# Optimization experiments

Hardware: AMD Instinct MI355X
Metric: run time of the kernel (lower is better)

## Reference

```python
import jax, jax.numpy as jnp
import numpy as np

B, T, N, D = 4, 8, 128, 512
H = 8
DH = D // H            # 64
HALF = DH // 2         # 32
NUM_FEATS = 3
SH_HID = 16
NUM_COEFF = 4          # l=0 (1) + l=1 (3)
ROPE_BASE = 1000.0
EPS = 1e-6
Y0 = 0.28209479177387814   # 1/sqrt(4*pi)
Y1 = 0.4886025119029199    # sqrt(3/(4*pi))


def setup_inputs() -> dict:
    key = jax.random.key(0)
    ks = jax.random.split(key, 16)
    s = 0.02
    return {
        'x_0': jax.random.normal(ks[0], (B, T, N, D), jnp.float32),
        'v_0': jax.random.normal(ks[1], (B, T, N, D), jnp.float32),
        'concatenated_features': jax.random.normal(ks[2], (B, T, N, D), jnp.float32),
        'q_data': jax.random.normal(ks[3], (B, T, N, D), jnp.float32),
        'Wq': jax.random.normal(ks[4], (D, D), jnp.float32) * s,
        'bq': jnp.zeros((D,), jnp.float32),
        'Wkv': jax.random.normal(ks[5], (NUM_FEATS, D, 2 * D), jnp.float32) * s,
        'bkv': jnp.zeros((NUM_FEATS, 2 * D), jnp.float32),
        'Wo': jax.random.normal(ks[6], (D, D), jnp.float32) * s,
        'bo': jnp.zeros((D,), jnp.float32),
        'feature_weights': jax.random.normal(ks[7], (NUM_FEATS,), jnp.float32) * 0.1,
        'attention_denom': jnp.full((H,), float(DH), jnp.float32),
        'W1': jax.random.normal(ks[8], (NUM_COEFF, SH_HID), jnp.float32) * 0.3,
        'b1': jnp.zeros((SH_HID,), jnp.float32),
        'W2': jax.random.normal(ks[9], (SH_HID, SH_HID), jnp.float32) * 0.3,
        'b2': jnp.zeros((SH_HID,), jnp.float32),
        'W3': jax.random.normal(ks[10], (SH_HID, H), jnp.float32) * 0.3,
        'b3': jnp.zeros((H,), jnp.float32),
    }


def _rope(t):
    # t: [B, H, S, DH]; groups of N nodes share the same timestep, offsets = 0
    positions = jnp.repeat(jnp.arange(T, dtype=jnp.float32), N)  # [S]
    freqs = 1.0 / (ROPE_BASE ** (2.0 * jnp.arange(HALF, dtype=jnp.float32) / DH))
    angle = positions[:, None] * freqs[None, :]                  # [S, HALF]
    cos_t, sin_t = jnp.cos(angle), jnp.sin(angle)
    t1, t2 = t[..., 0::2], t[..., 1::2]
    r0 = t1 * cos_t - t2 * sin_t
    r1 = t1 * sin_t + t2 * cos_t
    return jnp.stack([r0, r1], axis=-1).reshape(t.shape)


def _sh_bias(coords3, W1, b1, W2, b2, W3, b3):
    # coords3: [B, S, 3] -> bias [B, H, S, S]
    rel = coords3[:, :, None, :] - coords3[:, None, :, :]        # [B,S,S,3]
    norm = jnp.linalg.norm(rel, axis=-1, keepdims=True)
    unit = rel / (norm + EPS)
    # e3nn l=1 component order is (y, z, x)
    sh = jnp.concatenate([
        jnp.full(unit.shape[:-1] + (1,), Y0, unit.dtype),
        Y1 * unit[..., jnp.array([1, 2, 0])],
    ], axis=-1)                                                  # [B,S,S,4]
    h = jax.nn.silu(sh @ W1 + b1)
    h = jax.nn.silu(h @ W2 + b2)
    bias = h @ W3 + b3                                           # [B,S,S,H]
    return jnp.transpose(bias, (0, 3, 1, 2))                     # [B,H,S,S]


def reference(x_0, v_0, concatenated_features, q_data, Wq, bq, Wkv, bkv, Wo, bo,
              feature_weights, attention_denom, W1, b1, W2, b2, W3, b3):
    S = T * N
    q = (q_data.reshape(B, S, D) @ Wq + bq).reshape(B, S, H, DH)
    q = _rope(jnp.transpose(q, (0, 2, 1, 3)))                    # [B,H,S,DH]

    bias = _sh_bias(x_0[..., :3].reshape(B, S, 3), W1, b1, W2, b2, W3, b3)
    gates = jax.nn.softmax(feature_weights)
    inv_denom = (1.0 / attention_denom)[None, :, None, None]

    out = jnp.zeros((B, H, S, DH), q.dtype)
    for i, feat in enumerate([x_0, v_0, concatenated_features]):
        kv = feat.reshape(B, S, D) @ Wkv[i] + bkv[i]             # [B,S,2D]
        k, v = kv[..., :D], kv[..., D:]
        k = _rope(jnp.transpose(k.reshape(B, S, H, DH), (0, 2, 1, 3)))
        v = jnp.transpose(v.reshape(B, S, H, DH), (0, 2, 1, 3))
        scores = jnp.einsum('bhqd,bhkd->bhqk', q, k) * inv_denom + bias
        attn = jax.nn.softmax(scores, axis=-1)                   # dropout=identity (eval)
        out = out + gates[i] * jnp.einsum('bhqk,bhkd->bhqd', attn, v)

    out = jnp.transpose(out, (0, 2, 1, 3)).reshape(B, S, D)
    return (out @ Wo + bo).reshape(B, T, N, D)
```

## Files before the change

### kernel.cpp

```cpp
#include <hip/hip_runtime.h>
#include <hip/hip_bf16.h>

typedef unsigned short u16;
typedef __attribute__((ext_vector_type(4))) float f32x4;
typedef __attribute__((ext_vector_type(8))) short v8s;
typedef __attribute__((ext_vector_type(4))) _Float16 h16x4;
typedef __attribute__((ext_vector_type(2))) unsigned int u32x2;

#define NB 4
#define NT 8
#define NN 128
#define ND 512
#define NH 8
#define NDH 64
#define NS 1024

static __device__ __forceinline__ u16 f2b(float f) {
  __hip_bfloat16 h = __float2bfloat16(f);
  return *reinterpret_cast<u16*>(&h);
}
static __device__ __forceinline__ float b2f(u16 u) {
  __hip_bfloat16 h;
  *reinterpret_cast<u16*>(&h) = u;
  return __bfloat162float(h);
}
static __device__ __forceinline__ unsigned int cvtpk(float lo, float hi) {
  unsigned int r;
  asm("v_cvt_pk_bf16_f32 %0, %1, %2" : "=v"(r) : "v"(lo), "v"(hi));
  return r;
}
static __device__ __forceinline__ void gl16(const u16* g, u16* l) {
  __builtin_amdgcn_global_load_lds(
      (const __attribute__((address_space(1))) unsigned int*)g,
      (__attribute__((address_space(3))) unsigned int*)l, 16, 0, 0);
}
static __device__ __forceinline__ f32x4 mfma16(h16x4 a, h16x4 b, f32x4 c) {
#if __has_builtin(__builtin_amdgcn_mfma_f32_16x16x16f16)
  return __builtin_amdgcn_mfma_f32_16x16x16f16(a, b, c, 0, 0, 0);
#else
  f32x4 d;
  asm volatile("v_mfma_f32_16x16x16_f16 %0, %1, %2, %3\n\ts_nop 7\n\ts_nop 7"
               : "=v"(d)
               : "v"(a), "v"(b), "v"(c));
  return d;
#endif
}
static __device__ __forceinline__ float frcp(float x) { return __builtin_amdgcn_rcpf(x); }
static __device__ __forceinline__ float fsqrt(float x) { return __builtin_amdgcn_sqrtf(x); }

__global__ void __launch_bounds__(256) cast4_kernel(const float* __restrict__ s0,
                                                    const float* __restrict__ s1,
                                                    const float* __restrict__ s2,
                                                    const float* __restrict__ s3,
                                                    u16* __restrict__ dst) {
  int blk = blockIdx.x;
  int seg = blk >> 10;
  const float* src = seg == 0 ? s0 : (seg == 1 ? s1 : (seg == 2 ? s2 : s3));
  int i = (blk & 1023) * 256 + threadIdx.x;
  const float4* s4 = reinterpret_cast<const float4*>(src) + (size_t)i * 2;
  float4 a = s4[0], b = s4[1];
  u16 r[8] = {f2b(a.x), f2b(a.y), f2b(a.z), f2b(a.w),
              f2b(b.x), f2b(b.y), f2b(b.z), f2b(b.w)};
  *reinterpret_cast<v8s*>(dst + (size_t)seg * 2097152 + (size_t)i * 8) =
      *reinterpret_cast<v8s*>(r);
}

__global__ void __launch_bounds__(256) transpose_cast_kernel(const float* __restrict__ W,
                                                             u16* __restrict__ Wt,
                                                             int K, int N) {
  __shared__ float t[32][33];
  int tx = threadIdx.x & 31, ty = threadIdx.x >> 5;
  int kb = blockIdx.y * 32, nb = blockIdx.x * 32;
#pragma unroll
  for (int i = 0; i < 4; i++) {
    int r = ty + i * 8;
    t[r][tx] = W[(size_t)(kb + r) * N + nb + tx];
  }
  __syncthreads();
#pragma unroll
  for (int i = 0; i < 4; i++) {
    int r = ty + i * 8;
    Wt[(size_t)(nb + r) * K + kb + tx] = f2b(t[tx][r]);
  }
}

__global__ void coords_kernel(const float* __restrict__ x0, float* __restrict__ c, int n) {
  int i = blockIdx.x * blockDim.x + threadIdx.x;
  if (i < n) {
    float4 v;
    v.x = x0[(size_t)i * ND + 0];
    v.y = x0[(size_t)i * ND + 1];
    v.z = x0[(size_t)i * ND + 2];
    v.w = 0.0f;
    reinterpret_cast<float4*>(c)[i] = v;
  }
}

__global__ void __launch_bounds__(256) gemm_kernel(const u16* __restrict__ A,
                                                   const u16* __restrict__ Wt,
                                                   const float* __restrict__ bias,
                                                   const float* __restrict__ dnm,
                                                   u16* __restrict__ outK,
                                                   u16* __restrict__ outV,
                                                   float* __restrict__ outF,
                                                   int M, int N, int K, int mode, int f) {
  __shared__ __align__(16) u16 sbuf[2 * 8192];
  int nt = N >> 7;
  int by = blockIdx.x / nt, bx = blockIdx.x % nt;
  int tid = threadIdx.x;
  int lane = tid & 63, wave = tid >> 6;
  int g = lane >> 4, li = lane & 15;
  int wr = (wave & 1) * 64, wc = (wave >> 1) * 64;
  f32x4 acc[4][4] = {};
  const u16* srcs[4];
  int dsts[4];
#pragma unroll
  for (int j = 0; j < 4; j++) {
    int c = wave * 4 + j;
    if (c < 8)
      srcs[j] = A + (size_t)(by * 128 + c * 16 + li) * K + g * 8;
    else
      srcs[j] = Wt + (size_t)(bx * 128 + (c - 8) * 16 + li) * K + g * 8;
    dsts[j] = c * 512 + lane * 8;
  }
  int nsteps = K >> 5;
#pragma unroll
  for (int j = 0; j < 4; j++) gl16(srcs[j], sbuf + dsts[j]);
  for (int t = 0; t < nsteps; t++) {
    int p = t & 1;
    if (t < nsteps - 1) {
#pragma unroll
      for (int j = 0; j < 4; j++)
        gl16(srcs[j] + (t + 1) * 32, sbuf + (p ^ 1) * 8192 + dsts[j]);
      asm volatile("s_waitcnt vmcnt(4)" ::: "memory");
    } else {
      asm volatile("s_waitcnt vmcnt(0)" ::: "memory");
    }
    __builtin_amdgcn_s_barrier();
    __builtin_amdgcn_sched_barrier(0);
    const u16* bufb = sbuf + p * 8192;
    v8s a[4], b[4];
#pragma unroll
    for (int mi = 0; mi < 4; mi++)
      a[mi] = *reinterpret_cast<const v8s*>(bufb + ((wr >> 4) + mi) * 512 + lane * 8);
#pragma unroll
    for (int ni = 0; ni < 4; ni++)
      b[ni] = *reinterpret_cast<const v8s*>(bufb + 4096 + ((wc >> 4) + ni) * 512 + lane * 8);
    __builtin_amdgcn_s_setprio(1);
#pragma unroll
    for (int mi = 0; mi < 4; mi++)
#pragma unroll
      for (int ni = 0; ni < 4; ni++)
        acc[mi][ni] = __builtin_amdgcn_mfma_f32_16x16x32_bf16(a[mi], b[ni], acc[mi][ni], 0, 0, 0);
    __builtin_amdgcn_s_setprio(0);
    __builtin_amdgcn_s_barrier();
  }
#pragma unroll
  for (int mi = 0; mi < 4; mi++)
#pragma unroll
    for (int ni = 0; ni < 4; ni++) {
      int n = bx * 128 + wc + ni * 16 + li;
      float bn = bias[n];
      int mbase = by * 128 + wr + mi * 16 + 4 * g;
      bool isv = (mode == 1) && (n >= 512);
      if (mode == 2) {
#pragma unroll
        for (int r = 0; r < 4; r++)
          outF[(size_t)(mbase + r) * N + n] = acc[mi][ni][r] + bn;
      } else if (!isv) {
        int d = n & 63, h = (n & 511) >> 6;
        int j = d >> 1;
        float freq = __expf(-(float)j * 0.21586735246819178f);
        float sca = (mode == 0) ? frcp(dnm[h]) : 1.0f;
#pragma unroll
        for (int r = 0; r < 4; r++) {
          int mrow = mbase + r;
          int b = mrow >> 10, s = mrow & 1023;
          float val = acc[mi][ni][r] + bn;
          float partner = __shfl_xor(val, 1);
          float ang = (float)(s >> 7) * freq;
          float sn = __sinf(ang), cs = __cosf(ang);
          float res = (n & 1) ? (partner * sn + val * cs) : (val * cs - partner * sn);
          res *= sca;
          size_t idx;
          if (mode == 0)
            idx = ((size_t)(b * NH + h) * NS + s) * NDH + d;
          else
            idx = ((size_t)((f * NB + b) * NH + h) * NS + s) * NDH + d;
          outK[idx] = f2b(res);
        }
      } else {
        int vd = n - 512;
        int h = vd >> 6, d = vd & 63;
        int b = mbase >> 10, s0 = mbase & 1023;
        u16 pk[4];
#pragma unroll
        for (int r = 0; r < 4; r++) pk[r] = f2b(acc[mi][ni][r] + bn);
        u16* dst = outV + ((size_t)((f * NB + b) * NH + h) * NDH + d) * NS + s0;
        *reinterpret_cast<ushort4*>(dst) = *reinterpret_cast<ushort4*>(pk);
      }
    }
}

__global__ void __launch_bounds__(256) bias_kernel(const float* __restrict__ coords,
                                                   const float* __restrict__ W1,
                                                   const float* __restrict__ b1,
                                                   const float* __restrict__ W2,
                                                   const float* __restrict__ b2,
                                                   const float* __restrict__ W3,
                                                   const float* __restrict__ b3,
                                                   u16* __restrict__ biasF) {
  int wave = threadIdx.x >> 6, lane = threadIdx.x & 63;
  int g = lane >> 4, li = lane & 15;
  int id = blockIdx.x * 4 + wave;
  int kt = id & 31, qt = (id >> 5) & 63, b = id >> 11;
  const float Y0 = 0.28209479177387814f;
  const float Y1 = 0.4886025119029199f;

  h16x4 A1 = {}, A2, A3;
#pragma unroll
  for (int r = 0; r < 4; r++) {
    A1[r] = (g == 0) ? (_Float16)W1[r * 16 + li] : (_Float16)0.0f;
    A2[r] = (_Float16)W2[(4 * g + r) * 16 + li];
    A3[r] = (li < 8) ? (_Float16)W3[(4 * g + r) * 8 + li] : (_Float16)0.0f;
  }
  f32x4 b1g = reinterpret_cast<const f32x4*>(b1)[g];
  f32x4 b2g = reinterpret_cast<const f32x4*>(b2)[g];
  f32x4 b3g = {0.f, 0.f, 0.f, 0.f};
  if (g < 2) b3g = reinterpret_cast<const f32x4*>(b3)[g];

  const float4* crd4 = reinterpret_cast<const float4*>(coords);
  float4 cq = crd4[b * NS + qt * 16 + li];
  f32x4 zero = {0.f, 0.f, 0.f, 0.f};

  for (int gkc = 0; gkc < 4; gkc++) {
    unsigned int resw[4][4];
    float prev[4];
#pragma unroll
    for (int j = 0; j < 8; j++) {
      int k = kt * 32 + (j >> 2) * 16 + gkc * 4 + (j & 3);
      float4 ck = crd4[b * NS + k];
      float rx = cq.x - ck.x;
      float ry = cq.y - ck.y;
      float rz = cq.z - ck.z;
      float nrm = fsqrt(rx * rx + ry * ry + rz * rz);
      float inv = frcp(nrm + 1e-6f);
      h16x4 B1 = {};
      if (g == 0) {
        B1[0] = (_Float16)Y0;
        B1[1] = (_Float16)(Y1 * ry * inv);
        B1[2] = (_Float16)(Y1 * rz * inv);
        B1[3] = (_Float16)(Y1 * rx * inv);
      }
      f32x4 c1 = mfma16(A1, B1, zero);
      h16x4 B2;
#pragma unroll
      for (int r = 0; r < 4; r++) {
        float a = c1[r] + b1g[r];
        B2[r] = (_Float16)(a * frcp(1.0f + __expf(-a)));
      }
      f32x4 c2 = mfma16(A2, B2, zero);
      h16x4 B3;
#pragma unroll
      for (int r = 0; r < 4; r++) {
        float a = c2[r] + b2g[r];
        B3[r] = (_Float16)(a * frcp(1.0f + __expf(-a)));
      }
      f32x4 c3 = mfma16(A3, B3, zero);
#pragma unroll
      for (int r = 0; r < 4; r++) {
        float val = c3[r] + b3g[r];
        if (j & 1)
          resw[r][j >> 1] = cvtpk(prev[r], val);
        else
          prev[r] = val;
      }
    }
    if (g < 2) {
      size_t coff = ((size_t)(qt * 32 + kt) * 64 + gkc * 16 + li) * 8;
#pragma unroll
      for (int r = 0; r < 4; r++) {
        u16* dst = biasF + (size_t)(b * NH + 4 * g + r) * 1048576 + coff;
        *reinterpret_cast<uint4*>(dst) = *reinterpret_cast<uint4*>(resw[r]);
      }
    }
  }
}

#define ATTN_LDSB 12288
__global__ void __launch_bounds__(768, 6) attn_kernel(const u16* __restrict__ q,
                                                      const u16* __restrict__ kmat,
                                                      const u16* __restrict__ vt,
                                                      const u16* __restrict__ biasF,
                                                      const float* __restrict__ fw,
                                                      u16* __restrict__ attno) {
  __shared__ __align__(16) u16 sbuf[2 * ATTN_LDSB];
  int d = blockIdx.x;
  int x = d & 7, u = d >> 3;
  int bh = x * 4 + (u & 3);
  int qb = u >> 2;
  int h = bh & 7, b = bh >> 3;
  int wave = threadIdx.x >> 6, lane = threadIdx.x & 63;
  int g = lane >> 4, li = lane & 15;
  int ff = wave >> 2, qtl = wave & 3;
  int qt = qb * 4 + qtl;

  float f0 = fw[0], f1 = fw[1], f2v = fw[2];
  float mxg = fmaxf(fmaxf(f0, f1), f2v);
  float e0 = __expf(f0 - mxg), e1 = __expf(f1 - mxg), e2 = __expf(f2v - mxg);
  float es = e0 + e1 + e2;
  float gate = (ff == 0 ? e0 : (ff == 1 ? e1 : e2)) / es;

  const u16* qbase = q + ((size_t)bh * NS + qt * 16 + li) * NDH + g * 8;
  v8s qa0 = *reinterpret_cast<const v8s*>(qbase);
  v8s qa1 = *reinterpret_cast<const v8s*>(qbase + 32);
  const u16* bfrag = biasF + (size_t)bh * 1048576 + (size_t)qt * 16384;

  auto stage = [&](int kt, int p) {
    int k0 = kt * 32;
    u16* bufb = sbuf + p * ATTN_LDSB;
#pragma unroll
    for (int j = 0; j < 2; j++) {
      int c = wave * 2 + j;
      if (c < 12) {
        int cf = c >> 2, kks = (c >> 1) & 1, hf = c & 1;
        const u16* src = kmat + ((size_t)(cf * 32 + bh) * NS + k0 + kks * 16 + li) * NDH +
                         hf * 32 + g * 8;
        gl16(src, bufb + cf * 2048 + (c & 3) * 512 + lane * 8);
      } else {
        int cc = c - 12, cf = cc >> 2, ni = cc & 3;
        const u16* src = vt + ((size_t)(cf * 32 + bh) * NDH + ni * 16 + li) * NS + k0 + g * 8;
        gl16(src, bufb + 6144 + cf * 2048 + ni * 512 + lane * 8);
      }
    }
  };

  float m = 0.f;
  float lr = 0.f;
  f32x4 o[4] = {};
  f32x4 zero = {0.f, 0.f, 0.f, 0.f};
  int s0lane = ((g & 1) << 5) + li;
  int kksT = g >> 1;

  stage(0, 0);

  for (int t = 0; t < 32; t++) {
    int p = t & 1;
    v8s bb = *reinterpret_cast<const v8s*>(bfrag + ((size_t)t * 64 + lane) * 8);
    if (t < 31) {
      stage(t + 1, p ^ 1);
      asm volatile("s_waitcnt vmcnt(2)" ::: "memory");
    } else {
      asm volatile("s_waitcnt vmcnt(0)" ::: "memory");
    }
    __builtin_amdgcn_s_barrier();
    __builtin_amdgcn_sched_barrier(0);
    const u16* bufb = sbuf + p * ATTN_LDSB;
    v8s kf[2][2];
#pragma unroll
    for (int kks = 0; kks < 2; kks++)
#pragma unroll
      for (int hf = 0; hf < 2; hf++)
        kf[kks][hf] = *reinterpret_cast<const v8s*>(
            bufb + ff * 2048 + (kks * 2 + hf) * 512 + lane * 8);
    float pv[2][4];
    __builtin_amdgcn_s_setprio(1);
#pragma unroll
    for (int kks = 0; kks < 2; kks++) {
      f32x4 sc = __builtin_amdgcn_mfma_f32_16x16x32_bf16(kf[kks][0], qa0, zero, 0, 0, 0);
      sc = __builtin_amdgcn_mfma_f32_16x16x32_bf16(kf[kks][1], qa1, sc, 0, 0, 0);
#pragma unroll
      for (int r = 0; r < 4; r++)
        pv[kks][r] = sc[r] + b2f((u16)bb[kks * 4 + r]);
    }
    __builtin_amdgcn_s_setprio(0);
    float pmax = fmaxf(fmaxf(fmaxf(pv[0][0], pv[0][1]), pv[0][2]),
                       fmaxf(fmaxf(pv[0][3], pv[1][0]), pv[1][1]));
    pmax = fmaxf(fmaxf(pmax, pv[1][2]), pv[1][3]);
    if (!__all(pmax - m <= 8.0f)) {
      float rm = pmax;
      rm = fmaxf(rm, __shfl_xor(rm, 1));
      rm = fmaxf(rm, __shfl_xor(rm, 2));
      rm = fmaxf(rm, __shfl_xor(rm, 4));
      rm = fmaxf(rm, __shfl_xor(rm, 8));
      rm = fmaxf(rm, __shfl_xor(rm, 16));
      rm = fmaxf(rm, __shfl_xor(rm, 32));
      float sc2 = __expf(m - rm);
      lr *= sc2;
#pragma unroll
      for (int ni = 0; ni < 4; ni++)
#pragma unroll
        for (int r = 0; r < 4; r++) o[ni][r] *= sc2;
      m = rm;
    }
    float p2[2][4];
#pragma unroll
    for (int kks = 0; kks < 2; kks++)
#pragma unroll
      for (int r = 0; r < 4; r++) {
        p2[kks][r] = __expf(pv[kks][r] - m);
        lr += p2[kks][r];
      }
    unsigned int pA0 = cvtpk(p2[0][0], p2[0][1]);
    unsigned int pA1 = cvtpk(p2[0][2], p2[0][3]);
    unsigned int pB0 = cvtpk(p2[1][0], p2[1][1]);
    unsigned int pB1 = cvtpk(p2[1][2], p2[1][3]);
    int warr[4];
#if __has_builtin(__builtin_amdgcn_permlane32_swap) && \
    __has_builtin(__builtin_amdgcn_permlane16_swap)
    {
      u32x2 r0 = __builtin_amdgcn_permlane32_swap(pA0, pB0, false, false);
      u32x2 r1 = __builtin_amdgcn_permlane32_swap(pA1, pB1, false, false);
      u32x2 s0 = __builtin_amdgcn_permlane16_swap(r0[0], r0[1], false, false);
      u32x2 s1 = __builtin_amdgcn_permlane16_swap(r1[0], r1[1], false, false);
      warr[0] = s0[0];
      warr[1] = s1[0];
      warr[2] = s0[1];
      warr[3] = s1[1];
    }
#else
    {
      int a00 = __shfl((int)pA0, s0lane), a01 = __shfl((int)pA1, s0lane);
      int a10 = __shfl((int)pB0, s0lane), a11 = __shfl((int)pB1, s0lane);
      int c00 = __shfl((int)pA0, s0lane + 16), c01 = __shfl((int)pA1, s0lane + 16);
      int c10 = __shfl((int)pB0, s0lane + 16), c11 = __shfl((int)pB1, s0lane + 16);
      warr[0] = kksT ? a10 : a00;
      warr[1] = kksT ? a11 : a01;
      warr[2] = kksT ? c10 : c00;
      warr[3] = kksT ? c11 : c01;
    }
#endif
    v8s pa = *reinterpret_cast<v8s*>(warr);
    __builtin_amdgcn_s_setprio(1);
#pragma unroll
    for (int ni = 0; ni < 4; ni++) {
      v8s vb = *reinterpret_cast<const v8s*>(bufb + 6144 + ff * 2048 + ni * 512 + lane * 8);
      o[ni] = __builtin_amdgcn_mfma_f32_16x16x32_bf16(pa, vb, o[ni], 0, 0, 0);
    }
    __builtin_amdgcn_s_setprio(0);
    __builtin_amdgcn_s_barrier();
  }
  float l = lr;
  l += __shfl_xor(l, 16);
  l += __shfl_xor(l, 32);
  float scl = gate / l;
  float srow[4];
#pragma unroll
  for (int r = 0; r < 4; r++)
    srow[r] = __shfl(scl, (lane & 48) | (((lane >> 2) & 12) + r));
  float out[4][4];
#pragma unroll
  for (int ni = 0; ni < 4; ni++)
#pragma unroll
    for (int r = 0; r < 4; r++) out[ni][r] = o[ni][r] * srow[r];

  float* part = reinterpret_cast<float*>(sbuf);
  if (ff > 0) {
    int fq = (ff - 1) * 4 + qtl;
#pragma unroll
    for (int ni = 0; ni < 4; ni++)
#pragma unroll
      for (int r = 0; r < 4; r++)
        part[fq * 1088 + (4 * g + r) * 68 + ni * 16 + li] = out[ni][r];
  }
  __syncthreads();
  if (ff == 0) {
#pragma unroll
    for (int ni = 0; ni < 4; ni++)
#pragma unroll
      for (int r = 0; r < 4; r++) {
        float v = out[ni][r] + part[qtl * 1088 + (4 * g + r) * 68 + ni * 16 + li] +
                  part[(4 + qtl) * 1088 + (4 * g + r) * 68 + ni * 16 + li];
        attno[((size_t)(b * NS + qt * 16 + 4 * g + r)) * ND + h * NDH + ni * 16 + li] =
            f2b(v);
      }
  }
}

extern "C" void kernel_launch(void* const* d_in, const int* in_sizes, int n_in,
                              void* d_out, int out_size, void* d_ws, size_t ws_size,
                              hipStream_t stream) {
  const float* x0 = (const float*)d_in[0];
  const float* v0 = (const float*)d_in[1];
  const float* cf = (const float*)d_in[2];
  const float* qd = (const float*)d_in[3];
  const float* Wq = (const float*)d_in[4];
  const float* bq = (const float*)d_in[5];
  const float* Wkv = (const float*)d_in[6];
  const float* bkv = (const float*)d_in[7];
  const float* Wo = (const float*)d_in[8];
  const float* bo = (const float*)d_in[9];
  const float* fw = (const float*)d_in[10];
  const float* dnm = (const float*)d_in[11];
  const float* W1 = (const float*)d_in[12];
  const float* b1 = (const float*)d_in[13];
  const float* W2 = (const float*)d_in[14];
  const float* b2 = (const float*)d_in[15];
  const float* W3 = (const float*)d_in[16];
  const float* b3 = (const float*)d_in[17];

  char* ws = (char*)d_ws;
  size_t off = 0;
  auto alloc = [&](size_t bytes) -> void* {
    void* p = ws + off;
    off = (off + bytes + 255) & ~(size_t)255;
    return p;
  };
  const size_t E = 4096ull * 512;
  u16* Aq = (u16*)alloc(E * 2);
  u16* Af = (u16*)alloc(3 * E * 2);
  u16* Wqt = (u16*)alloc(262144ull * 2);
  u16* Wkvt = (u16*)alloc(3ull * 524288 * 2);
  u16* Wot = (u16*)alloc(262144ull * 2);
  float* crd = (float*)alloc(4096ull * 4 * 4);
  u16* qr = (u16*)alloc(E * 2);
  u16* kr = (u16*)alloc(3 * E * 2);
  u16* vtr = (u16*)alloc(3 * E * 2);
  u16* biasF = (u16*)alloc(33554432ull * 2);
  u16* attno = (u16*)alloc(E * 2);
  (void)ws_size; (void)in_sizes; (void)n_in; (void)out_size; (void)Af;

  cast4_kernel<<<4096, 256, 0, stream>>>(qd, x0, v0, cf, Aq);
  coords_kernel<<<16, 256, 0, stream>>>(x0, crd, 4096);
  dim3 tg1(16, 16);
  transpose_cast_kernel<<<tg1, 256, 0, stream>>>(Wq, Wqt, 512, 512);
  dim3 tg2(32, 16);
  for (int f = 0; f < 3; f++)
    transpose_cast_kernel<<<tg2, 256, 0, stream>>>(Wkv + (size_t)f * 524288,
                                                   Wkvt + (size_t)f * 524288, 512, 1024);
  transpose_cast_kernel<<<tg1, 256, 0, stream>>>(Wo, Wot, 512, 512);

  gemm_kernel<<<128, 256, 0, stream>>>(Aq, Wqt, bq, dnm, qr, nullptr, nullptr,
                                       4096, 512, 512, 0, 0);
  for (int f = 0; f < 3; f++)
    gemm_kernel<<<256, 256, 0, stream>>>(Af + (size_t)f * E, Wkvt + (size_t)f * 524288,
                                         bkv + f * 1024, nullptr, kr, vtr, nullptr,
                                         4096, 1024, 512, 1, f);
  bias_kernel<<<2048, 256, 0, stream>>>(crd, W1, b1, W2, b2, W3, b3, biasF);
  attn_kernel<<<512, 768, 0, stream>>>(qr, kr, vtr, biasF, fw, attno);
  gemm_kernel<<<128, 256, 0, stream>>>(attno, Wot, bo, nullptr, nullptr, nullptr,
                                       (float*)d_out, 4096, 512, 512, 2, 0);
}
```

Baseline: 216.0 us.

## Merge prep and KV GEMM launches, fold log2e scaling, fuse bias into MFMA

Merges the coords extraction into the cast kernel and the five weight transposes into one launch. The three KV projection GEMMs now run as a single launch of 768 blocks. Folds log2(e) into the query scale and the SH bias MLP output so the attention softmax can use exp2 directly. The attention kernel also feeds the bias in as the MFMA accumulator init, uses rsqrt for the SH normalization, and raises the rescale threshold to match the log2 domain. The aim is fewer kernel launches, better GPU fill for the KV GEMM, and fewer softmax ALU ops, at the cost of slightly different numerics (rsq with clamp instead of 1/(sqrt+eps), bias values scaled by log2e before being stored as bf16).

```diff
diff --git a/kernel.cpp b/kernel.cpp
--- a/kernel.cpp
+++ b/kernel.cpp
@@ -14,6 +14,7 @@
 #define NH 8
 #define NDH 64
 #define NS 1024
+#define LOG2E 1.4426950408889634f
 
 static __device__ __forceinline__ u16 f2b(float f) {
   __hip_bfloat16 h = __float2bfloat16(f);
@@ -46,14 +47,25 @@
 #endif
 }
 static __device__ __forceinline__ float frcp(float x) { return __builtin_amdgcn_rcpf(x); }
-static __device__ __forceinline__ float fsqrt(float x) { return __builtin_amdgcn_sqrtf(x); }
 
 __global__ void __launch_bounds__(256) cast4_kernel(const float* __restrict__ s0,
                                                     const float* __restrict__ s1,
                                                     const float* __restrict__ s2,
                                                     const float* __restrict__ s3,
-                                                    u16* __restrict__ dst) {
+                                                    u16* __restrict__ dst,
+                                                    float* __restrict__ crd) {
   int blk = blockIdx.x;
+  if (blk >= 4096) {
+    for (int i = threadIdx.x; i < 4096; i += 256) {
+      float4 v;
+      v.x = s1[(size_t)i * ND + 0];
+      v.y = s1[(size_t)i * ND + 1];
+      v.z = s1[(size_t)i * ND + 2];
+      v.w = 0.0f;
+      reinterpret_cast<float4*>(crd)[i] = v;
+    }
+    return;
+  }
   int seg = blk >> 10;
   const float* src = seg == 0 ? s0 : (seg == 1 ? s1 : (seg == 2 ? s2 : s3));
   int i = (blk & 1023) * 256 + threadIdx.x;
@@ -65,12 +77,31 @@
       *reinterpret_cast<v8s*>(r);
 }
 
-__global__ void __launch_bounds__(256) transpose_cast_kernel(const float* __restrict__ W,
-                                                             u16* __restrict__ Wt,
-                                                             int K, int N) {
+__global__ void __launch_bounds__(256) transpose_all_kernel(const float* __restrict__ Wq,
+                                                            const float* __restrict__ Wkv,
+                                                            const float* __restrict__ Wo,
+                                                            u16* __restrict__ Wqt,
+                                                            u16* __restrict__ Wkvt,
+                                                            u16* __restrict__ Wot) {
   __shared__ float t[32][33];
+  int bid = blockIdx.x;
+  const float* W;
+  u16* Wt;
+  int N, tt;
+  if (bid < 256) {
+    W = Wq; Wt = Wqt; N = 512; tt = bid;
+  } else if (bid < 1792) {
+    int f = (bid - 256) >> 9;
+    tt = (bid - 256) & 511;
+    W = Wkv + (size_t)f * 524288;
+    Wt = Wkvt + (size_t)f * 524288;
+    N = 1024;
+  } else {
+    W = Wo; Wt = Wot; N = 512; tt = bid - 1792;
+  }
+  int ntb = N >> 5;
+  int nb = (tt % ntb) * 32, kb = (tt / ntb) * 32;
   int tx = threadIdx.x & 31, ty = threadIdx.x >> 5;
-  int kb = blockIdx.y * 32, nb = blockIdx.x * 32;
 #pragma unroll
   for (int i = 0; i < 4; i++) {
     int r = ty + i * 8;
@@ -80,19 +111,7 @@
 #pragma unroll
   for (int i = 0; i < 4; i++) {
     int r = ty + i * 8;
-    Wt[(size_t)(nb + r) * K + kb + tx] = f2b(t[tx][r]);
-  }
-}
-
-__global__ void coords_kernel(const float* __restrict__ x0, float* __restrict__ c, int n) {
-  int i = blockIdx.x * blockDim.x + threadIdx.x;
-  if (i < n) {
-    float4 v;
-    v.x = x0[(size_t)i * ND + 0];
-    v.y = x0[(size_t)i * ND + 1];
-    v.z = x0[(size_t)i * ND + 2];
-    v.w = 0.0f;
-    reinterpret_cast<float4*>(c)[i] = v;
+    Wt[(size_t)(nb + r) * 512 + kb + tx] = f2b(t[tx][r]);
   }
 }
 
@@ -105,8 +124,16 @@
                                                    float* __restrict__ outF,
                                                    int M, int N, int K, int mode, int f) {
   __shared__ __align__(16) u16 sbuf[2 * 8192];
+  int bid = blockIdx.x;
+  if (mode == 1) {
+    f = bid >> 8;
+    bid &= 255;
+    A += (size_t)f * 2097152;
+    Wt += (size_t)f * 524288;
+    bias += f * 1024;
+  }
   int nt = N >> 7;
-  int by = blockIdx.x / nt, bx = blockIdx.x % nt;
+  int by = bid / nt, bx = bid % nt;
   int tid = threadIdx.x;
   int lane = tid & 63, wave = tid >> 6;
   int g = lane >> 4, li = lane & 15;
@@ -171,7 +198,7 @@
         int d = n & 63, h = (n & 511) >> 6;
         int j = d >> 1;
         float freq = __expf(-(float)j * 0.21586735246819178f);
-        float sca = (mode == 0) ? frcp(dnm[h]) : 1.0f;
+        float sca = (mode == 0) ? frcp(dnm[h]) * LOG2E : 1.0f;
 #pragma unroll
         for (int r = 0; r < 4; r++) {
           int mrow = mbase + r;
@@ -222,12 +249,12 @@
   for (int r = 0; r < 4; r++) {
     A1[r] = (g == 0) ? (_Float16)W1[r * 16 + li] : (_Float16)0.0f;
     A2[r] = (_Float16)W2[(4 * g + r) * 16 + li];
-    A3[r] = (li < 8) ? (_Float16)W3[(4 * g + r) * 8 + li] : (_Float16)0.0f;
+    A3[r] = (li < 8) ? (_Float16)(W3[(4 * g + r) * 8 + li] * LOG2E) : (_Float16)0.0f;
   }
   f32x4 b1g = reinterpret_cast<const f32x4*>(b1)[g];
   f32x4 b2g = reinterpret_cast<const f32x4*>(b2)[g];
   f32x4 b3g = {0.f, 0.f, 0.f, 0.f};
-  if (g < 2) b3g = reinterpret_cast<const f32x4*>(b3)[g];
+  if (g < 2) b3g = reinterpret_cast<const f32x4*>(b3)[g] * LOG2E;
 
   const float4* crd4 = reinterpret_cast<const float4*>(coords);
   float4 cq = crd4[b * NS + qt * 16 + li];
@@ -243,8 +270,8 @@
       float rx = cq.x - ck.x;
       float ry = cq.y - ck.y;
       float rz = cq.z - ck.z;
-      float nrm = fsqrt(rx * rx + ry * ry + rz * rz);
-      float inv = frcp(nrm + 1e-6f);
+      float d2 = rx * rx + ry * ry + rz * rz;
+      float inv = __builtin_amdgcn_rsqf(fmaxf(d2, 1e-20f));
       h16x4 B1 = {};
       if (g == 0) {
         B1[0] = (_Float16)Y0;
@@ -338,7 +365,6 @@
   float m = 0.f;
   float lr = 0.f;
   f32x4 o[4] = {};
-  f32x4 zero = {0.f, 0.f, 0.f, 0.f};
   int s0lane = ((g & 1) << 5) + li;
   int kksT = g >> 1;
 
@@ -363,21 +389,23 @@
       for (int hf = 0; hf < 2; hf++)
         kf[kks][hf] = *reinterpret_cast<const v8s*>(
             bufb + ff * 2048 + (kks * 2 + hf) * 512 + lane * 8);
-    float pv[2][4];
+    f32x4 bc[2];
+#pragma unroll
+    for (int kks = 0; kks < 2; kks++)
+#pragma unroll
+      for (int r = 0; r < 4; r++) bc[kks][r] = b2f((u16)bb[kks * 4 + r]);
+    f32x4 pv[2];
     __builtin_amdgcn_s_setprio(1);
 #pragma unroll
     for (int kks = 0; kks < 2; kks++) {
-      f32x4 sc = __builtin_amdgcn_mfma_f32_16x16x32_bf16(kf[kks][0], qa0, zero, 0, 0, 0);
-      sc = __builtin_amdgcn_mfma_f32_16x16x32_bf16(kf[kks][1], qa1, sc, 0, 0, 0);
-#pragma unroll
-      for (int r = 0; r < 4; r++)
-        pv[kks][r] = sc[r] + b2f((u16)bb[kks * 4 + r]);
+      f32x4 sc = __builtin_amdgcn_mfma_f32_16x16x32_bf16(kf[kks][0], qa0, bc[kks], 0, 0, 0);
+      pv[kks] = __builtin_amdgcn_mfma_f32_16x16x32_bf16(kf[kks][1], qa1, sc, 0, 0, 0);
     }
     __builtin_amdgcn_s_setprio(0);
     float pmax = fmaxf(fmaxf(fmaxf(pv[0][0], pv[0][1]), pv[0][2]),
                        fmaxf(fmaxf(pv[0][3], pv[1][0]), pv[1][1]));
     pmax = fmaxf(fmaxf(pmax, pv[1][2]), pv[1][3]);
-    if (!__all(pmax - m <= 8.0f)) {
+    if (!__all(pmax - m <= 11.0f)) {
       float rm = pmax;
       rm = fmaxf(rm, __shfl_xor(rm, 1));
       rm = fmaxf(rm, __shfl_xor(rm, 2));
@@ -385,7 +413,7 @@
       rm = fmaxf(rm, __shfl_xor(rm, 8));
       rm = fmaxf(rm, __shfl_xor(rm, 16));
       rm = fmaxf(rm, __shfl_xor(rm, 32));
-      float sc2 = __expf(m - rm);
+      float sc2 = exp2f(m - rm);
       lr *= sc2;
 #pragma unroll
       for (int ni = 0; ni < 4; ni++)
@@ -398,7 +426,7 @@
     for (int kks = 0; kks < 2; kks++)
 #pragma unroll
       for (int r = 0; r < 4; r++) {
-        p2[kks][r] = __expf(pv[kks][r] - m);
+        p2[kks][r] = exp2f(pv[kks][r] - m);
         lr += p2[kks][r];
       }
     unsigned int pA0 = cvtpk(p2[0][0], p2[0][1]);
@@ -520,22 +548,13 @@
   u16* attno = (u16*)alloc(E * 2);
   (void)ws_size; (void)in_sizes; (void)n_in; (void)out_size; (void)Af;
 
-  cast4_kernel<<<4096, 256, 0, stream>>>(qd, x0, v0, cf, Aq);
-  coords_kernel<<<16, 256, 0, stream>>>(x0, crd, 4096);
-  dim3 tg1(16, 16);
-  transpose_cast_kernel<<<tg1, 256, 0, stream>>>(Wq, Wqt, 512, 512);
-  dim3 tg2(32, 16);
-  for (int f = 0; f < 3; f++)
-    transpose_cast_kernel<<<tg2, 256, 0, stream>>>(Wkv + (size_t)f * 524288,
-                                                   Wkvt + (size_t)f * 524288, 512, 1024);
-  transpose_cast_kernel<<<tg1, 256, 0, stream>>>(Wo, Wot, 512, 512);
+  cast4_kernel<<<4097, 256, 0, stream>>>(qd, x0, v0, cf, Aq, crd);
+  transpose_all_kernel<<<2048, 256, 0, stream>>>(Wq, Wkv, Wo, Wqt, Wkvt, Wot);
 
   gemm_kernel<<<128, 256, 0, stream>>>(Aq, Wqt, bq, dnm, qr, nullptr, nullptr,
                                        4096, 512, 512, 0, 0);
-  for (int f = 0; f < 3; f++)
-    gemm_kernel<<<256, 256, 0, stream>>>(Af + (size_t)f * E, Wkvt + (size_t)f * 524288,
-                                         bkv + f * 1024, nullptr, kr, vtr, nullptr,
-                                         4096, 1024, 512, 1, f);
+  gemm_kernel<<<768, 256, 0, stream>>>(Af, Wkvt, bkv, nullptr, kr, vtr, nullptr,
+                                       4096, 1024, 512, 1, 0);
   bias_kernel<<<2048, 256, 0, stream>>>(crd, W1, b1, W2, b2, W3, b3, biasF);
   attn_kernel<<<512, 768, 0, stream>>>(qr, kr, vtr, biasF, fw, attno);
   gemm_kernel<<<128, 256, 0, stream>>>(attno, Wot, bo, nullptr, nullptr, nullptr,
```

After: 202.4 us. -6.3%, faster.
